# Performance work log

Measured on AMD Instinct MI355X. Metric: run time of the kernel, lower is better.

The kernel has to match this reference:

```python
import jax, jax.numpy as jnp
import numpy as np
import math

D_MODEL = 512
D_K = 64
B, S = 8, 2048
NEG_INF = -1.0e9


def setup_inputs() -> dict:
    key = jax.random.key(0)
    ks = jax.random.split(key, 10)
    inp = {
        "query_source": jax.random.normal(ks[0], (B, S, D_MODEL), dtype=jnp.float32),
        "key_source": jax.random.normal(ks[1], (B, S, D_MODEL), dtype=jnp.float32),
        "value_source": jax.random.normal(ks[2], (B, S, D_MODEL), dtype=jnp.float32),
        # causal mask: 1 means "masked" (future positions), matching masked_fill(mask == 1, -1e9)
        "mask": jnp.triu(jnp.ones((S, S), dtype=jnp.int32), k=1),
        # Linear weights stored as [in, out] so x @ W + b matches torch Linear
        "Wq": jax.random.normal(ks[3], (D_MODEL, D_K), dtype=jnp.float32) / math.sqrt(D_MODEL),
        "bq": jax.random.normal(ks[4], (D_K,), dtype=jnp.float32) * 0.01,
        "Wk": jax.random.normal(ks[5], (D_MODEL, D_K), dtype=jnp.float32) / math.sqrt(D_MODEL),
        "bk": jax.random.normal(ks[6], (D_K,), dtype=jnp.float32) * 0.01,
        "Wv": jax.random.normal(ks[7], (D_MODEL, D_K), dtype=jnp.float32) / math.sqrt(D_MODEL),
        "bv": jax.random.normal(ks[8], (D_K,), dtype=jnp.float32) * 0.01,
    }
    return inp


def reference(query_source, key_source, value_source, mask, Wq, bq, Wk, bk, Wv, bv):
    d_k = Wq.shape[-1]
    Q = query_source @ Wq + bq          # [B, S, d_k]
    K = key_source @ Wk + bk            # [B, S, d_k]
    V = value_source @ Wv + bv          # [B, S, d_k]
    scores = jnp.einsum("bqd,bkd->bqk", Q, K) / jnp.sqrt(jnp.float32(d_k))  # [B, S, S]
    scores = jnp.where(mask == 1, jnp.float32(NEG_INF), scores)
    attn = jax.nn.softmax(scores, axis=-1)
    return jnp.einsum("bqk,bkd->bqd", attn, V)  # [B, S, d_k]
```

## Files before the change

### kernel.cpp

```cpp
#include <hip/hip_runtime.h>

#define BATCH 8
#define SEQ 2048
#define DMODEL 512
#define DK 64

typedef __attribute__((ext_vector_type(8))) short short8;
typedef __attribute__((ext_vector_type(4))) float f32x4;

__device__ __forceinline__ unsigned f2bfbits(float f) {
  unsigned u = __builtin_bit_cast(unsigned, f);
  return (u + 0x7FFFu + ((u >> 16) & 1u)) >> 16;
}

__device__ __forceinline__ void glds16(const void* g, void* l) {
  __builtin_amdgcn_global_load_lds(
      (const __attribute__((address_space(1))) unsigned int*)g,
      (__attribute__((address_space(3))) unsigned int*)l, 16, 0, 0);
}

#define MFMA_BF16(a, b, c) __builtin_amdgcn_mfma_f32_16x16x32_bf16((a), (b), (c), 0, 0, 0)

__global__ __launch_bounds__(256) void wtrans_kernel(
    const float* __restrict__ Wq, const float* __restrict__ Wk,
    const float* __restrict__ Wv, unsigned short* __restrict__ Wt)
{
  const int p = blockIdx.y;
  const float* W = (p == 0) ? Wq : (p == 1) ? Wk : Wv;
  const int t = threadIdx.x;
  const int c = t & 63;
  const int k0 = blockIdx.x * 64 + (t >> 6) * 16;
  unsigned short* dst = Wt + (p * 64 + c) * 512;
  #pragma unroll
  for (int i = 0; i < 16; ++i) {
    int k = k0 + i;
    dst[k] = (unsigned short)f2bfbits(W[k * 64 + c]);
  }
}

__global__ __launch_bounds__(256) void proj_kernel(
    const float* __restrict__ Xq, const float* __restrict__ Xk, const float* __restrict__ Xv,
    const unsigned short* __restrict__ Wt,
    const float* __restrict__ bq, const float* __restrict__ bk, const float* __restrict__ bv,
    unsigned short* __restrict__ oq, unsigned short* __restrict__ ok,
    unsigned short* __restrict__ ov)
{
  const int p = blockIdx.y;
  const float* X    = (p == 0) ? Xq : (p == 1) ? Xk : Xv;
  const float* bias = (p == 0) ? bq : (p == 1) ? bk : bv;
  unsigned short* out = (p == 0) ? oq : (p == 1) ? ok : ov;
  const float scale = (p == 0) ? 0.125f : 1.0f;
  const unsigned short* Wtp = Wt + p * 64 * 512;

  const int tid = threadIdx.x;
  const long row0 = (long)blockIdx.x * 64;
  const int w = tid >> 6, lane = tid & 63, m = lane & 15, quad = lane >> 4;

  const float* xp = X + (row0 + w * 16 + m) * DMODEL + quad * 8;
  const unsigned short* wp = Wtp + m * 512 + quad * 8;

  f32x4 acc[4];
  #pragma unroll
  for (int c = 0; c < 4; ++c) acc[c] = (f32x4){0.f, 0.f, 0.f, 0.f};

  #pragma unroll
  for (int s = 0; s < 16; ++s) {
    float4 v0 = *(const float4*)(xp + s * 32);
    float4 v1 = *(const float4*)(xp + s * 32 + 4);
    uint4 pk;
    pk.x = f2bfbits(v0.x) | (f2bfbits(v0.y) << 16);
    pk.y = f2bfbits(v0.z) | (f2bfbits(v0.w) << 16);
    pk.z = f2bfbits(v1.x) | (f2bfbits(v1.y) << 16);
    pk.w = f2bfbits(v1.z) | (f2bfbits(v1.w) << 16);
    const short8 aF = __builtin_bit_cast(short8, pk);
    #pragma unroll
    for (int c = 0; c < 4; ++c) {
      const short8 bF = *(const short8*)(wp + (c * 16) * 512 + s * 32);
      acc[c] = MFMA_BF16(aF, bF, acc[c]);
    }
  }

  float bbv[4];
  #pragma unroll
  for (int c = 0; c < 4; ++c) bbv[c] = bias[c * 16 + m];

  if (p < 2) {
    #pragma unroll
    for (int c = 0; c < 4; ++c) {
      #pragma unroll
      for (int r = 0; r < 4; ++r) {
        long row = row0 + w * 16 + quad * 4 + r;
        float v = (acc[c][r] + bbv[c]) * scale;
        out[row * DK + c * 16 + m] = (unsigned short)f2bfbits(v);
      }
    }
  } else {
    long b = row0 >> 11;
    int sbase = (int)(row0 & 2047) + w * 16 + quad * 4;
    #pragma unroll
    for (int c = 0; c < 4; ++c) {
      unsigned lo = f2bfbits(acc[c][0] + bbv[c]) | (f2bfbits(acc[c][1] + bbv[c]) << 16);
      unsigned hi = f2bfbits(acc[c][2] + bbv[c]) | (f2bfbits(acc[c][3] + bbv[c]) << 16);
      *(uint2*)(out + ((long)(b * 64 + c * 16 + m)) * SEQ + sbase) = make_uint2(lo, hi);
    }
  }
}

__global__ __launch_bounds__(256) void attn_kernel(
    const unsigned short* __restrict__ Qb,
    const unsigned short* __restrict__ Kb,
    const unsigned short* __restrict__ Vtg,
    unsigned short* __restrict__ Opart,
    float* __restrict__ lpart,
    float* __restrict__ out)
{
  __shared__ __attribute__((aligned(16))) short ks[2][64 * 64];
  __shared__ __attribute__((aligned(16))) short vt[2][64 * 64];
  __shared__ __attribute__((aligned(16))) short ps[4][16 * 72];

  const int tid = threadIdx.x;
  const int bi = blockIdx.x & 7;
  const int j = blockIdx.x >> 3;

  int qt = 0, c = 0;
  {
    int jj = j;
    for (qt = 0; qt < 32; ++qt) {
      int cnt = (qt >> 2) + 1;
      if (jj < cnt) { c = jj; break; }
      jj -= cnt;
    }
  }
  const int q0 = qt << 6;
  const int kt0 = c << 2;
  const int ntc = min(4, qt + 1 - (c << 2));

  const int w = tid >> 6, lane = tid & 63, m = lane & 15, quad = lane >> 4;
  const int xm = m & 7;

  const int qrow = q0 + w * 16 + m;
  const unsigned short* qp = Qb + ((long)(bi * SEQ + qrow)) * DK + quad * 8;
  const short8 qA0 = *(const short8*)qp;
  const short8 qA1 = *(const short8*)(qp + 32);

  f32x4 o[4];
  #pragma unroll
  for (int d = 0; d < 4; ++d) o[d] = (f32x4){0.f, 0.f, 0.f, 0.f};
  float psum[4] = {0.f, 0.f, 0.f, 0.f};

  const int srow = lane >> 3;
  const int slc  = (lane & 7) ^ srow;

  auto stage = [&](int buf, int ktg) {
    const int k0 = ktg << 6;
    #pragma unroll
    for (int t = 0; t < 2; ++t) {
      const int row = w * 16 + t * 8 + srow;
      glds16(Kb + ((long)(bi * SEQ + k0 + row)) * DK + slc * 8,
             &ks[buf][(w * 16 + t * 8) * 64]);
      glds16(Vtg + ((long)(bi * DK + row)) * SEQ + k0 + slc * 8,
             &vt[buf][(w * 16 + t * 8) * 64]);
    }
  };

  stage(0, kt0);

  for (int i = 0; i < ntc; ++i) {
    __syncthreads();
    if (i + 1 < ntc) stage((i + 1) & 1, kt0 + i + 1);

    const int ktg = kt0 + i;
    const short* ksb = &ks[i & 1][0];
    const short* vtb = &vt[i & 1][0];

    f32x4 sc[4];
    #pragma unroll
    for (int cc = 0; cc < 4; ++cc) {
      const short* kr = ksb + (cc * 16 + m) * 64;
      f32x4 a = {0.f, 0.f, 0.f, 0.f};
      a = MFMA_BF16(qA0, *(const short8*)(kr + ((quad ^ xm) * 8)), a);
      a = MFMA_BF16(qA1, *(const short8*)(kr + (((4 + quad) ^ xm) * 8)), a);
      sc[cc] = a;
    }

    if (ktg == qt) {
      const int rb = q0 + w * 16 + quad * 4;
      const int k0g = ktg << 6;
      #pragma unroll
      for (int cc = 0; cc < 4; ++cc) {
        const int col = k0g + cc * 16 + m;
        #pragma unroll
        for (int r = 0; r < 4; ++r)
          if (col > rb + r) sc[cc][r] = -1e9f;
      }
    }

    #pragma unroll
    for (int cc = 0; cc < 4; ++cc) {
      #pragma unroll
      for (int r = 0; r < 4; ++r)
        sc[cc][r] = __expf(sc[cc][r]);
    }
    #pragma unroll
    for (int r = 0; r < 4; ++r)
      psum[r] += (sc[0][r] + sc[1][r]) + (sc[2][r] + sc[3][r]);

    short* pw = &ps[w][0];
    #pragma unroll
    for (int cc = 0; cc < 4; ++cc) {
      #pragma unroll
      for (int r = 0; r < 4; ++r)
        pw[(quad * 4 + r) * 72 + cc * 16 + m] = (short)f2bfbits(sc[cc][r]);
    }
    asm volatile("s_waitcnt lgkmcnt(0)" ::: "memory");

    const short8 pA0 = *(const short8*)(pw + m * 72 + quad * 8);
    const short8 pA1 = *(const short8*)(pw + m * 72 + quad * 8 + 32);

    #pragma unroll
    for (int d = 0; d < 4; ++d) {
      const short* vr = vtb + (d * 16 + m) * 64;
      o[d] = MFMA_BF16(pA0, *(const short8*)(vr + ((quad ^ xm) * 8)), o[d]);
      o[d] = MFMA_BF16(pA1, *(const short8*)(vr + (((4 + quad) ^ xm) * 8)), o[d]);
    }
  }

  #pragma unroll
  for (int off = 1; off < 16; off <<= 1) {
    #pragma unroll
    for (int r = 0; r < 4; ++r)
      psum[r] += __shfl_xor(psum[r], off);
  }

  const int rb = w * 16 + quad * 4;
  if (qt < 4) {
    #pragma unroll
    for (int r = 0; r < 4; ++r) {
      const float inv = 1.0f / psum[r];
      float* op = out + ((long)(bi * SEQ + q0 + rb + r)) * DK + m;
      op[0]  = o[0][r] * inv;
      op[16] = o[1][r] * inv;
      op[32] = o[2][r] * inv;
      op[48] = o[3][r] * inv;
    }
  } else {
    const int pi = bi * 144 + j;
    unsigned short* opp = Opart + (long)pi * 4096;
    #pragma unroll
    for (int r = 0; r < 4; ++r) {
      unsigned short* op = opp + (rb + r) * 64 + m;
      op[0]  = (unsigned short)f2bfbits(o[0][r]);
      op[16] = (unsigned short)f2bfbits(o[1][r]);
      op[32] = (unsigned short)f2bfbits(o[2][r]);
      op[48] = (unsigned short)f2bfbits(o[3][r]);
    }
    if (m == 0) {
      #pragma unroll
      for (int r = 0; r < 4; ++r)
        lpart[pi * 64 + rb + r] = psum[r];
    }
  }
}

__global__ __launch_bounds__(256) void combine_kernel(
    const unsigned short* __restrict__ Opart, const float* __restrict__ lpart,
    float* __restrict__ out)
{
  const int bi = blockIdx.x & 7;
  const int qt = (blockIdx.x >> 3) + 4;
  const int g = qt >> 2, r = qt & 3;
  const int base = bi * 144 + (g + 1) * (2 * g + r);
  const int cnt = g + 1;

  __shared__ float linv[64];
  const int tid = threadIdx.x;
  if (tid < 64) {
    float s = 0.f;
    for (int i = 0; i < cnt; ++i) s += lpart[(base + i) * 64 + tid];
    linv[tid] = 1.0f / s;
  }
  __syncthreads();

  const int row = tid >> 2;
  const int col0 = (tid & 3) << 4;
  float a[16];
  #pragma unroll
  for (int k = 0; k < 16; ++k) a[k] = 0.f;

  for (int i = 0; i < cnt; ++i) {
    const uint4* op = (const uint4*)(Opart + (long)(base + i) * 4096 + row * 64 + col0);
    uint4 t0 = op[0], t1 = op[1];
    const unsigned uu[8] = {t0.x, t0.y, t0.z, t0.w, t1.x, t1.y, t1.z, t1.w};
    #pragma unroll
    for (int k = 0; k < 8; ++k) {
      a[2 * k]     += __builtin_bit_cast(float, uu[k] << 16);
      a[2 * k + 1] += __builtin_bit_cast(float, uu[k] & 0xFFFF0000u);
    }
  }

  const float inv = linv[row];
  float4* dst = (float4*)(out + ((long)(bi * SEQ + (qt << 6) + row)) * DK + col0);
  #pragma unroll
  for (int k = 0; k < 4; ++k)
    dst[k] = make_float4(a[4*k] * inv, a[4*k+1] * inv, a[4*k+2] * inv, a[4*k+3] * inv);
}

extern "C" void kernel_launch(void* const* d_in, const int* in_sizes, int n_in,
                              void* d_out, int out_size, void* d_ws, size_t ws_size,
                              hipStream_t stream) {
  const float* qs   = (const float*)d_in[0];
  const float* ksrc = (const float*)d_in[1];
  const float* vsrc = (const float*)d_in[2];
  const float* Wq = (const float*)d_in[4];
  const float* bq = (const float*)d_in[5];
  const float* Wk = (const float*)d_in[6];
  const float* bk = (const float*)d_in[7];
  const float* Wv = (const float*)d_in[8];
  const float* bv = (const float*)d_in[9];

  unsigned short* Qb  = (unsigned short*)d_ws;
  unsigned short* Kb  = Qb + (long)BATCH * SEQ * DK;
  unsigned short* Vtg = Kb + (long)BATCH * SEQ * DK;
  unsigned short* Opart = Vtg + (long)BATCH * SEQ * DK;
  float* lpart = (float*)(Opart + (long)1152 * 64 * 64);
  unsigned short* Wtg = (unsigned short*)d_out;
  float* outp = (float*)d_out;

  wtrans_kernel<<<dim3(8, 3), dim3(256), 0, stream>>>(Wq, Wk, Wv, Wtg);
  proj_kernel<<<dim3(256, 3), dim3(256), 0, stream>>>(
      qs, ksrc, vsrc, Wtg, bq, bk, bv, Qb, Kb, Vtg);
  attn_kernel<<<dim3(1152), dim3(256), 0, stream>>>(Qb, Kb, Vtg, Opart, lpart, outp);
  combine_kernel<<<dim3(224), dim3(256), 0, stream>>>(Opart, lpart, outp);
}
```

Baseline: 187.3 us.

## Stage projection weights in swizzled LDS, prefetch X rows, split combine blocks

The projection kernel now copies the whole bf16 weight slice (64x512) into XOR-swizzled shared memory with async global-to-LDS loads, instead of every wave fetching B fragments straight from global memory. It also keeps a four-step register ring of upcoming X float4 loads to hide global latency. The combine kernel is split into four times as many 64-thread blocks, each handling 16 rows, to spread work over more CUs. The cost is 64 KB of LDS per projection block, which limits occupancy, plus a sync before the MFMA loop.

```diff
diff --git a/kernel.cpp b/kernel.cpp
--- a/kernel.cpp
+++ b/kernel.cpp
@@ -45,6 +45,8 @@
     unsigned short* __restrict__ oq, unsigned short* __restrict__ ok,
     unsigned short* __restrict__ ov)
 {
+  __shared__ __attribute__((aligned(16))) short wt[64 * 512];
+
   const int p = blockIdx.y;
   const float* X    = (p == 0) ? Xq : (p == 1) ? Xk : Xv;
   const float* bias = (p == 0) ? bq : (p == 1) ? bk : bv;
@@ -55,27 +57,50 @@
   const int tid = threadIdx.x;
   const long row0 = (long)blockIdx.x * 64;
   const int w = tid >> 6, lane = tid & 63, m = lane & 15, quad = lane >> 4;
+  const int xm = m & 7;
 
   const float* xp = X + (row0 + w * 16 + m) * DMODEL + quad * 8;
-  const unsigned short* wp = Wtp + m * 512 + quad * 8;
+
+  float4 v0[4], v1[4];
+  #pragma unroll
+  for (int s = 0; s < 4; ++s) {
+    v0[s] = *(const float4*)(xp + s * 32);
+    v1[s] = *(const float4*)(xp + s * 32 + 4);
+  }
+
+  #pragma unroll
+  for (int i = 0; i < 16; ++i) {
+    const int u = i * 256 + tid;
+    const int row = u >> 6;
+    const int g = (u & 63) ^ (row & 7);
+    glds16(Wtp + row * 512 + g * 8, &wt[u * 8]);
+  }
 
   f32x4 acc[4];
   #pragma unroll
   for (int c = 0; c < 4; ++c) acc[c] = (f32x4){0.f, 0.f, 0.f, 0.f};
 
+  __syncthreads();
+
   #pragma unroll
   for (int s = 0; s < 16; ++s) {
-    float4 v0 = *(const float4*)(xp + s * 32);
-    float4 v1 = *(const float4*)(xp + s * 32 + 4);
+    const int slot = s & 3;
     uint4 pk;
-    pk.x = f2bfbits(v0.x) | (f2bfbits(v0.y) << 16);
-    pk.y = f2bfbits(v0.z) | (f2bfbits(v0.w) << 16);
-    pk.z = f2bfbits(v1.x) | (f2bfbits(v1.y) << 16);
-    pk.w = f2bfbits(v1.z) | (f2bfbits(v1.w) << 16);
+    pk.x = f2bfbits(v0[slot].x) | (f2bfbits(v0[slot].y) << 16);
+    pk.y = f2bfbits(v0[slot].z) | (f2bfbits(v0[slot].w) << 16);
+    pk.z = f2bfbits(v1[slot].x) | (f2bfbits(v1[slot].y) << 16);
+    pk.w = f2bfbits(v1[slot].z) | (f2bfbits(v1[slot].w) << 16);
     const short8 aF = __builtin_bit_cast(short8, pk);
+
+    if (s + 4 < 16) {
+      v0[slot] = *(const float4*)(xp + (s + 4) * 32);
+      v1[slot] = *(const float4*)(xp + (s + 4) * 32 + 4);
+    }
+
     #pragma unroll
     for (int c = 0; c < 4; ++c) {
-      const short8 bF = *(const short8*)(wp + (c * 16) * 512 + s * 32);
+      const int ch = ((s * 4 + quad) ^ xm) * 8;
+      const short8 bF = *(const short8*)&wt[(c * 16 + m) * 512 + ch];
       acc[c] = MFMA_BF16(aF, bF, acc[c]);
     }
   }
@@ -262,26 +287,28 @@
   }
 }
 
-__global__ __launch_bounds__(256) void combine_kernel(
+__global__ __launch_bounds__(64) void combine_kernel(
     const unsigned short* __restrict__ Opart, const float* __restrict__ lpart,
     float* __restrict__ out)
 {
   const int bi = blockIdx.x & 7;
-  const int qt = (blockIdx.x >> 3) + 4;
-  const int g = qt >> 2, r = qt & 3;
-  const int base = bi * 144 + (g + 1) * (2 * g + r);
+  const int t = blockIdx.x >> 3;
+  const int qt = (t >> 2) + 4;
+  const int qr = t & 3;
+  const int g = qt >> 2, rr = qt & 3;
+  const int base = bi * 144 + (g + 1) * (2 * g + rr);
   const int cnt = g + 1;
 
-  __shared__ float linv[64];
+  __shared__ float linv[16];
   const int tid = threadIdx.x;
-  if (tid < 64) {
+  if (tid < 16) {
     float s = 0.f;
-    for (int i = 0; i < cnt; ++i) s += lpart[(base + i) * 64 + tid];
+    for (int i = 0; i < cnt; ++i) s += lpart[(base + i) * 64 + qr * 16 + tid];
     linv[tid] = 1.0f / s;
   }
   __syncthreads();
 
-  const int row = tid >> 2;
+  const int row = qr * 16 + (tid >> 2);
   const int col0 = (tid & 3) << 4;
   float a[16];
   #pragma unroll
@@ -298,7 +325,7 @@
     }
   }
 
-  const float inv = linv[row];
+  const float inv = linv[tid >> 2];
   float4* dst = (float4*)(out + ((long)(bi * SEQ + (qt << 6) + row)) * DK + col0);
   #pragma unroll
   for (int k = 0; k < 4; ++k)
@@ -330,5 +357,5 @@
   proj_kernel<<<dim3(256, 3), dim3(256), 0, stream>>>(
       qs, ksrc, vsrc, Wtg, bq, bk, bv, Qb, Kb, Vtg);
   attn_kernel<<<dim3(1152), dim3(256), 0, stream>>>(Qb, Kb, Vtg, Opart, lpart, outp);
-  combine_kernel<<<dim3(224), dim3(256), 0, stream>>>(Opart, lpart, outp);
-}
+  combine_kernel<<<dim3(896), dim3(64), 0, stream>>>(Opart, lpart, outp);
+}
```

Measured after the change: 181.5 us. 3.1% less time.
